# Performance work log

Hardware: AMD Instinct MI355X
Metric: run time of the kernel (lower is better)

## Reference

```python
import jax, jax.numpy as jnp
import numpy as np

NUM_CODE = 1024
CODE_DIM = 256
COMMITMENT_COST = 0.25
EPS = 1e-12


def _l2norm(v, axis=-1):
    n = jnp.sqrt(jnp.sum(v * v, axis=axis, keepdims=True))
    return v / jnp.maximum(n, EPS)


def setup_inputs() -> dict:
    key = jax.random.key(0)
    k1, k2 = jax.random.split(key)
    x = jax.random.normal(k1, (64, 8, 128, CODE_DIM), dtype=jnp.float32)
    # codebook init: uniform(-1/num_code, 1/num_code) as in torch
    cw = (jax.random.uniform(k2, (NUM_CODE, CODE_DIM), dtype=jnp.float32) * 2.0 - 1.0) / NUM_CODE
    return {"x": x, "codebook_weight": cw}


def reference(x, codebook_weight):
    # x: [B, C, T, D]
    xn = _l2norm(x)                              # normalized encoder output
    cb = _l2norm(codebook_weight)                # [N, D] normalized codebook
    # cosine similarity and nearest-code lookup
    sim = jnp.einsum('bctd,nd->bctn', xn, cb)    # [B, C, T, N]
    code_indices = jnp.argmax(sim, axis=-1)      # [B, C, T] int
    # one-hot @ codebook == direct gather of normalized codebook rows
    quantized = cb[code_indices]                 # [B, C, T, D]
    # VQ losses (both inputs already normalized, matching torch detach semantics in fwd value)
    e_latent = jnp.mean((quantized - xn) ** 2)
    q_latent = jnp.mean((quantized - xn) ** 2)
    loss = q_latent + COMMITMENT_COST * e_latent
    # straight-through estimator (forward value == quantized)
    quantized_st = xn + jax.lax.stop_gradient(quantized - xn)
    # perplexity from code usage histogram (mean of one-hot over B,C,T)
    total = code_indices.size
    counts = jnp.zeros((NUM_CODE,), jnp.float32).at[code_indices.reshape(-1)].add(1.0)
    avg_probs = counts / total
    perplexity = jnp.exp(-jnp.sum(avg_probs * jnp.log(avg_probs + 1e-10)))
    return (loss, quantized_st, perplexity, codebook_weight, code_indices)
```

## Files before the change

### kernel.cpp

```cpp
#include <hip/hip_runtime.h>
#include <math.h>

#define D 256
#define NCODE 1024
#define EPSF 1e-12f
#define ROWS 32
#define LSTR 260
#define SLABK 8
#define NSLAB 128

#define GLOAD_LDS16(gp, lp) \
  __builtin_amdgcn_global_load_lds( \
      (const __attribute__((address_space(1))) unsigned int*)(const void*)(gp), \
      (__attribute__((address_space(3))) unsigned int*)(void*)(lp), 16, 0, 0)



__global__ __launch_bounds__(256) void normalize_cb(const float* __restrict__ w,
                                                    float* __restrict__ cb_n,
                                                    float* __restrict__ cb_t) {
    const int wave = threadIdx.x >> 6;
    const int lane = threadIdx.x & 63;
    const int row  = blockIdx.x * 4 + wave;
    float4 wv = *(const float4*)(w + (size_t)row * D + lane * 4);
    float s = wv.x * wv.x + wv.y * wv.y + wv.z * wv.z + wv.w * wv.w;
    #pragma unroll
    for (int off = 32; off; off >>= 1) s += __shfl_xor(s, off);
    const float scale = 1.0f / fmaxf(sqrtf(s), EPSF);
    float4 o;
    o.x = wv.x * scale; o.y = wv.y * scale; o.z = wv.z * scale; o.w = wv.w * scale;
    *(float4*)(cb_n + (size_t)row * D + lane * 4) = o;
    const int k = lane * 4;
    cb_t[(size_t)(k + 0) * NCODE + row] = o.x;
    cb_t[(size_t)(k + 1) * NCODE + row] = o.y;
    cb_t[(size_t)(k + 2) * NCODE + row] = o.z;
    cb_t[(size_t)(k + 3) * NCODE + row] = o.w;
}

__global__ __launch_bounds__(256, 3) void vq_main(const float* __restrict__ x,
                                                  const float* __restrict__ cb_t,
                                                  int* __restrict__ idx_ws,
                                                  unsigned int* __restrict__ counts,
                                                  float* __restrict__ loss_acc,
                                                  float* __restrict__ out_idx_f) {
    __shared__ float xl[ROWS * LSTR];
    __shared__ float bl[2][SLABK * 256];
    __shared__ float nrm_s[ROWS];
    const int tid  = threadIdx.x;
    const int wave = tid >> 6;
    const int lane = tid & 63;
    const int v0   = blockIdx.x * ROWS;

    const float4* xg = (const float4*)(x + (size_t)v0 * D);
    #pragma unroll
    for (int i = 0; i < 8; ++i) {
        const int f  = tid + i * 256;
        const int m  = f >> 6;
        const int kk = (f & 63) << 2;
        float4 val = xg[f];
        *(float4*)&xl[m * LSTR + kk] = val;
    }
    __syncthreads();

    {
        const float* g = cb_t + (size_t)(wave * 2) * NCODE + lane * 4;
        GLOAD_LDS16(g,         &bl[0][(wave * 2 + 0) * 256]);
        GLOAD_LDS16(g + NCODE, &bl[0][(wave * 2 + 1) * 256]);
    }

    {
        const int row = tid >> 3, part = tid & 7;
        float ss = 0.f;
        #pragma unroll
        for (int q = 0; q < 8; ++q) {
            float4 xv = *(const float4*)&xl[row * LSTR + part * 32 + q * 4];
            ss += xv.x * xv.x + xv.y * xv.y + xv.z * xv.z + xv.w * xv.w;
        }
        ss += __shfl_xor(ss, 1);
        ss += __shfl_xor(ss, 2);
        ss += __shfl_xor(ss, 4);
        if (part == 0) nrm_s[row] = fmaxf(sqrtf(ss), EPSF);
    }
    __syncthreads();

    const int tn = tid & 31, tm = tid >> 5;
    float best[4]; int bidx[4];
    #pragma unroll
    for (int i = 0; i < 4; ++i) { best[i] = -3.4e38f; bidx[i] = 0; }

    float acc[4][8];
    #pragma unroll
    for (int i = 0; i < 4; ++i)
        #pragma unroll
        for (int j = 0; j < 8; ++j) acc[i][j] = 0.f;

    const float* xrow0 = &xl[(tm * 4 + 0) * LSTR];
    const float* xrow1 = &xl[(tm * 4 + 1) * LSTR];
    const float* xrow2 = &xl[(tm * 4 + 2) * LSTR];
    const float* xrow3 = &xl[(tm * 4 + 3) * LSTR];

    #pragma unroll 1
    for (int s = 0; s < NSLAB; ++s) {
        if (s) __syncthreads();

        if (s + 1 < NSLAB) {
            const int c1  = (s + 1) >> 5;
            const int k01 = ((s + 1) & 31) * SLABK;
            float* dst = bl[(s + 1) & 1];
            const float* g = cb_t + (size_t)(k01 + wave * 2) * NCODE + c1 * 256 + lane * 4;
            GLOAD_LDS16(g,         dst + (wave * 2 + 0) * 256);
            GLOAD_LDS16(g + NCODE, dst + (wave * 2 + 1) * 256);
        }

        const float* btn = &bl[s & 1][tn * 8];
        const int kx0 = (s & 31) * SLABK;
        #pragma unroll
        for (int k4 = 0; k4 < 2; ++k4) {
            float4 xa0 = *(const float4*)(xrow0 + kx0 + k4 * 4);
            float4 xa1 = *(const float4*)(xrow1 + kx0 + k4 * 4);
            float4 xa2 = *(const float4*)(xrow2 + kx0 + k4 * 4);
            float4 xa3 = *(const float4*)(xrow3 + kx0 + k4 * 4);
            #pragma unroll
            for (int kk = 0; kk < 4; ++kk) {
                const float* bk = btn + (k4 * 4 + kk) * 256;
                float4 b0 = *(const float4*)bk;
                float4 b1 = *(const float4*)(bk + 4);
                const float xv0 = ((const float*)&xa0)[kk];
                const float xv1 = ((const float*)&xa1)[kk];
                const float xv2 = ((const float*)&xa2)[kk];
                const float xv3 = ((const float*)&xa3)[kk];
                float xv[4] = {xv0, xv1, xv2, xv3};
                #pragma unroll
                for (int i = 0; i < 4; ++i) {
                    acc[i][0] = fmaf(xv[i], b0.x, acc[i][0]);
                    acc[i][1] = fmaf(xv[i], b0.y, acc[i][1]);
                    acc[i][2] = fmaf(xv[i], b0.z, acc[i][2]);
                    acc[i][3] = fmaf(xv[i], b0.w, acc[i][3]);
                    acc[i][4] = fmaf(xv[i], b1.x, acc[i][4]);
                    acc[i][5] = fmaf(xv[i], b1.y, acc[i][5]);
                    acc[i][6] = fmaf(xv[i], b1.z, acc[i][6]);
                    acc[i][7] = fmaf(xv[i], b1.w, acc[i][7]);
                }
            }
        }

        if ((s & 31) == 31) {
            const int n0 = (s >> 5) * 256 + tn * 8;
            #pragma unroll
            for (int i = 0; i < 4; ++i)
                #pragma unroll
                for (int j = 0; j < 8; ++j) {
                    if (acc[i][j] > best[i]) { best[i] = acc[i][j]; bidx[i] = n0 + j; }
                    acc[i][j] = 0.f;
                }
        }
    }

    #pragma unroll
    for (int off = 16; off; off >>= 1) {
        #pragma unroll
        for (int i = 0; i < 4; ++i) {
            float ov = __shfl_xor(best[i], off);
            int   oi = __shfl_xor(bidx[i], off);
            if (ov > best[i] || (ov == best[i] && oi < bidx[i])) { best[i] = ov; bidx[i] = oi; }
        }
    }

    float lpart = 0.f;
    if (tn == 0) {
        #pragma unroll
        for (int i = 0; i < 4; ++i) {
            const int row = tm * 4 + i;
            const int v   = v0 + row;
            const float sim = best[i] / nrm_s[row];
            lpart += 2.f - 2.f * sim;
            idx_ws[v] = bidx[i];
            out_idx_f[v] = (float)bidx[i];
            atomicAdd(&counts[bidx[i]], 1u);
        }
    }
    #pragma unroll
    for (int off = 32; off; off >>= 1) lpart += __shfl_xor(lpart, off);
    if ((tid & 63) == 0) atomicAdd(loss_acc, lpart);
}

__global__ __launch_bounds__(256) void gather_q(const int* __restrict__ idx_ws,
                                                const float* __restrict__ cb_n,
                                                float* __restrict__ outq) {
    const int wave = threadIdx.x >> 6;
    const int lane = threadIdx.x & 63;
    const int v = blockIdx.x * 4 + wave;
    const int idx = idx_ws[v];
    float4 val = *(const float4*)(cb_n + (size_t)idx * D + lane * 4);
    *(float4*)(outq + (size_t)v * D + lane * 4) = val;
}

__global__ __launch_bounds__(1024) void finalize(const unsigned int* __restrict__ counts,
                                                 const float* __restrict__ loss_acc,
                                                 float* __restrict__ out_loss,
                                                 float* __restrict__ out_perp) {
    __shared__ float red[16];
    const int t = threadIdx.x;
    const float p = (float)counts[t] / 65536.0f;
    float term = p * logf(p + 1e-10f);
    #pragma unroll
    for (int off = 32; off; off >>= 1) term += __shfl_xor(term, off);
    if ((t & 63) == 0) red[t >> 6] = term;
    __syncthreads();
    if (t < 16) {
        float s = red[t];
        #pragma unroll
        for (int off = 8; off; off >>= 1) s += __shfl_xor(s, off);
        if (t == 0) {
            *out_perp = expf(-s);
            *out_loss = 1.25f * (*loss_acc) / 16777216.0f;
        }
    }
}

extern "C" void kernel_launch(void* const* d_in, const int* in_sizes, int n_in,
                              void* d_out, int out_size, void* d_ws, size_t ws_size,
                              hipStream_t stream) {
    const float* x  = (const float*)d_in[0];
    const float* cw = (const float*)d_in[1];
    float* out = (float*)d_out;
    float* ws  = (float*)d_ws;

    float* cb_n          = ws;
    float* cb_t          = ws + 262144;
    int* idx_ws          = (int*)(ws + 524288);
    unsigned int* counts = (unsigned int*)(ws + 589824);
    float* loss_acc      = ws + 590848;

    hipMemsetAsync(counts, 0, (1024 + 1) * sizeof(float), stream);

    normalize_cb<<<256, 256, 0, stream>>>(cw, cb_n, cb_t);
    vq_main<<<2048, 256, 0, stream>>>(x, cb_t, idx_ws, counts, loss_acc,
                                      out + 17039362);
    gather_q<<<16384, 256, 0, stream>>>(idx_ws, cb_n, out + 1);
    finalize<<<1, 1024, 0, stream>>>(counts, loss_acc, out, out + 16777217);
    hipMemcpyAsync(out + 16777218, cw, (size_t)NCODE * D * sizeof(float),
                   hipMemcpyDeviceToDevice, stream);
}
```

Baseline: 587.7 us.

## Halve codebook slab depth, remap column ownership, compute norms in registers

Shrinks each codebook slab from 8 to 4 k-rows and doubles the number of slabs. Each thread now owns two strided groups of 4 codes (tn*4 and tn*4+128) instead of 8 contiguous ones, which changes the LDS read pattern so a wavefront's b-loads are contiguous. The x tile drops its padding and row norms move from shared memory into per-thread registers. LDS shrinks enough to raise the occupancy hint from 3 to 4 blocks per CU, at the cost of twice as many barriers per block.

```diff
diff --git a/kernel.cpp b/kernel.cpp
--- a/kernel.cpp
+++ b/kernel.cpp
@@ -5,9 +5,8 @@
 #define NCODE 1024
 #define EPSF 1e-12f
 #define ROWS 32
-#define LSTR 260
-#define SLABK 8
-#define NSLAB 128
+#define SLABK 4
+#define NSLAB 256
 
 #define GLOAD_LDS16(gp, lp) \
   __builtin_amdgcn_global_load_lds( \
@@ -37,15 +36,14 @@
     cb_t[(size_t)(k + 3) * NCODE + row] = o.w;
 }
 
-__global__ __launch_bounds__(256, 3) void vq_main(const float* __restrict__ x,
+__global__ __launch_bounds__(256, 4) void vq_main(const float* __restrict__ x,
                                                   const float* __restrict__ cb_t,
                                                   int* __restrict__ idx_ws,
                                                   unsigned int* __restrict__ counts,
                                                   float* __restrict__ loss_acc,
                                                   float* __restrict__ out_idx_f) {
-    __shared__ float xl[ROWS * LSTR];
+    __shared__ float xl[ROWS * 256];
     __shared__ float bl[2][SLABK * 256];
-    __shared__ float nrm_s[ROWS];
     const int tid  = threadIdx.x;
     const int wave = tid >> 6;
     const int lane = tid & 63;
@@ -54,36 +52,36 @@
     const float4* xg = (const float4*)(x + (size_t)v0 * D);
     #pragma unroll
     for (int i = 0; i < 8; ++i) {
-        const int f  = tid + i * 256;
-        const int m  = f >> 6;
-        const int kk = (f & 63) << 2;
+        const int f = tid + i * 256;
         float4 val = xg[f];
-        *(float4*)&xl[m * LSTR + kk] = val;
+        *(float4*)&xl[f * 4] = val;
     }
     __syncthreads();
 
     {
-        const float* g = cb_t + (size_t)(wave * 2) * NCODE + lane * 4;
-        GLOAD_LDS16(g,         &bl[0][(wave * 2 + 0) * 256]);
-        GLOAD_LDS16(g + NCODE, &bl[0][(wave * 2 + 1) * 256]);
-    }
-
-    {
-        const int row = tid >> 3, part = tid & 7;
-        float ss = 0.f;
-        #pragma unroll
-        for (int q = 0; q < 8; ++q) {
-            float4 xv = *(const float4*)&xl[row * LSTR + part * 32 + q * 4];
-            ss += xv.x * xv.x + xv.y * xv.y + xv.z * xv.z + xv.w * xv.w;
-        }
+        const float* g = cb_t + (size_t)wave * NCODE + lane * 4;
+        GLOAD_LDS16(g, &bl[0][wave * 256]);
+    }
+
+    const int tn = tid & 31, tm = tid >> 5;
+
+    float nrm[4];
+    #pragma unroll
+    for (int i = 0; i < 4; ++i) {
+        const float* xr = &xl[(tm * 4 + i) * 256];
+        float4 a = *(const float4*)(xr + tn * 4);
+        float4 b = *(const float4*)(xr + 128 + tn * 4);
+        float ss = a.x * a.x + a.y * a.y + a.z * a.z + a.w * a.w
+                 + b.x * b.x + b.y * b.y + b.z * b.z + b.w * b.w;
+        ss += __shfl_xor(ss, 16);
+        ss += __shfl_xor(ss, 8);
+        ss += __shfl_xor(ss, 4);
+        ss += __shfl_xor(ss, 2);
         ss += __shfl_xor(ss, 1);
-        ss += __shfl_xor(ss, 2);
-        ss += __shfl_xor(ss, 4);
-        if (part == 0) nrm_s[row] = fmaxf(sqrtf(ss), EPSF);
+        nrm[i] = fmaxf(sqrtf(ss), EPSF);
     }
     __syncthreads();
 
-    const int tn = tid & 31, tm = tid >> 5;
     float best[4]; int bidx[4];
     #pragma unroll
     for (int i = 0; i < 4; ++i) { best[i] = -3.4e38f; bidx[i] = 0; }
@@ -94,65 +92,66 @@
         #pragma unroll
         for (int j = 0; j < 8; ++j) acc[i][j] = 0.f;
 
-    const float* xrow0 = &xl[(tm * 4 + 0) * LSTR];
-    const float* xrow1 = &xl[(tm * 4 + 1) * LSTR];
-    const float* xrow2 = &xl[(tm * 4 + 2) * LSTR];
-    const float* xrow3 = &xl[(tm * 4 + 3) * LSTR];
+    const float* xrow0 = &xl[(tm * 4 + 0) * 256];
+    const float* xrow1 = &xl[(tm * 4 + 1) * 256];
+    const float* xrow2 = &xl[(tm * 4 + 2) * 256];
+    const float* xrow3 = &xl[(tm * 4 + 3) * 256];
 
     #pragma unroll 1
     for (int s = 0; s < NSLAB; ++s) {
         if (s) __syncthreads();
 
         if (s + 1 < NSLAB) {
-            const int c1  = (s + 1) >> 5;
-            const int k01 = ((s + 1) & 31) * SLABK;
-            float* dst = bl[(s + 1) & 1];
-            const float* g = cb_t + (size_t)(k01 + wave * 2) * NCODE + c1 * 256 + lane * 4;
-            GLOAD_LDS16(g,         dst + (wave * 2 + 0) * 256);
-            GLOAD_LDS16(g + NCODE, dst + (wave * 2 + 1) * 256);
-        }
-
-        const float* btn = &bl[s & 1][tn * 8];
-        const int kx0 = (s & 31) * SLABK;
-        #pragma unroll
-        for (int k4 = 0; k4 < 2; ++k4) {
-            float4 xa0 = *(const float4*)(xrow0 + kx0 + k4 * 4);
-            float4 xa1 = *(const float4*)(xrow1 + kx0 + k4 * 4);
-            float4 xa2 = *(const float4*)(xrow2 + kx0 + k4 * 4);
-            float4 xa3 = *(const float4*)(xrow3 + kx0 + k4 * 4);
+            const int sn = s + 1;
+            const int c1 = sn >> 6;
+            const int k1 = ((sn & 63) << 2) + wave;
+            const float* g = cb_t + (size_t)k1 * NCODE + c1 * 256 + lane * 4;
+            GLOAD_LDS16(g, &bl[sn & 1][wave * 256]);
+        }
+
+        const float* bs = &bl[s & 1][tn * 4];
+        const int kx0 = (s & 63) << 2;
+        float4 xa0 = *(const float4*)(xrow0 + kx0);
+        float4 xa1 = *(const float4*)(xrow1 + kx0);
+        float4 xa2 = *(const float4*)(xrow2 + kx0);
+        float4 xa3 = *(const float4*)(xrow3 + kx0);
+        #pragma unroll
+        for (int kk = 0; kk < 4; ++kk) {
+            float4 b0 = *(const float4*)(bs + kk * 256);
+            float4 b1 = *(const float4*)(bs + kk * 256 + 128);
+            const float xv0 = ((const float*)&xa0)[kk];
+            const float xv1 = ((const float*)&xa1)[kk];
+            const float xv2 = ((const float*)&xa2)[kk];
+            const float xv3 = ((const float*)&xa3)[kk];
+            float xv[4] = {xv0, xv1, xv2, xv3};
             #pragma unroll
-            for (int kk = 0; kk < 4; ++kk) {
-                const float* bk = btn + (k4 * 4 + kk) * 256;
-                float4 b0 = *(const float4*)bk;
-                float4 b1 = *(const float4*)(bk + 4);
-                const float xv0 = ((const float*)&xa0)[kk];
-                const float xv1 = ((const float*)&xa1)[kk];
-                const float xv2 = ((const float*)&xa2)[kk];
-                const float xv3 = ((const float*)&xa3)[kk];
-                float xv[4] = {xv0, xv1, xv2, xv3};
+            for (int i = 0; i < 4; ++i) {
+                acc[i][0] = fmaf(xv[i], b0.x, acc[i][0]);
+                acc[i][1] = fmaf(xv[i], b0.y, acc[i][1]);
+                acc[i][2] = fmaf(xv[i], b0.z, acc[i][2]);
+                acc[i][3] = fmaf(xv[i], b0.w, acc[i][3]);
+                acc[i][4] = fmaf(xv[i], b1.x, acc[i][4]);
+                acc[i][5] = fmaf(xv[i], b1.y, acc[i][5]);
+                acc[i][6] = fmaf(xv[i], b1.z, acc[i][6]);
+                acc[i][7] = fmaf(xv[i], b1.w, acc[i][7]);
+            }
+        }
+
+        if ((s & 63) == 63) {
+            const int n0 = (s >> 6) * 256 + tn * 4;
+            #pragma unroll
+            for (int i = 0; i < 4; ++i) {
                 #pragma unroll
-                for (int i = 0; i < 4; ++i) {
-                    acc[i][0] = fmaf(xv[i], b0.x, acc[i][0]);
-                    acc[i][1] = fmaf(xv[i], b0.y, acc[i][1]);
-                    acc[i][2] = fmaf(xv[i], b0.z, acc[i][2]);
-                    acc[i][3] = fmaf(xv[i], b0.w, acc[i][3]);
-                    acc[i][4] = fmaf(xv[i], b1.x, acc[i][4]);
-                    acc[i][5] = fmaf(xv[i], b1.y, acc[i][5]);
-                    acc[i][6] = fmaf(xv[i], b1.z, acc[i][6]);
-                    acc[i][7] = fmaf(xv[i], b1.w, acc[i][7]);
-                }
-            }
-        }
-
-        if ((s & 31) == 31) {
-            const int n0 = (s >> 5) * 256 + tn * 8;
-            #pragma unroll
-            for (int i = 0; i < 4; ++i)
-                #pragma unroll
-                for (int j = 0; j < 8; ++j) {
+                for (int j = 0; j < 4; ++j) {
                     if (acc[i][j] > best[i]) { best[i] = acc[i][j]; bidx[i] = n0 + j; }
                     acc[i][j] = 0.f;
                 }
+                #pragma unroll
+                for (int j = 4; j < 8; ++j) {
+                    if (acc[i][j] > best[i]) { best[i] = acc[i][j]; bidx[i] = n0 + 128 + (j - 4); }
+                    acc[i][j] = 0.f;
+                }
+            }
         }
     }
 
@@ -172,7 +171,7 @@
         for (int i = 0; i < 4; ++i) {
             const int row = tm * 4 + i;
             const int v   = v0 + row;
-            const float sim = best[i] / nrm_s[row];
+            const float sim = best[i] / nrm[i];
             lpart += 2.f - 2.f * sim;
             idx_ws[v] = bidx[i];
             out_idx_f[v] = (float)bidx[i];
```

Measured after the change: 583.0 us. Within noise of the previous version (-0.8%).
